# Kernel tuning notes

Hardware: AMD Instinct MI355X
Metric: run time of the kernel (lower is better)

The kernel has to match this reference:

```python
import jax, jax.numpy as jnp
import numpy as np

B, N, DIMS, K, UNITS = 4, 16384, 2, 16, 128
K1 = K + 1
CH = (DIMS + 1) * K1 + DIMS  # 53, matches ch_dims in LocSE.build
EPS = 1e-8


def setup_inputs() -> dict:
    key = jax.random.key(0)
    k1, k2, k3, k4 = jax.random.split(key, 4)
    pc = jax.random.normal(k1, (B, N, DIMS), jnp.float32)
    feats = jax.random.normal(k2, (B, N, UNITS // 2), jnp.float32)
    n_idx = jax.random.randint(k3, (B, N, K1), 0, N).astype(jnp.int32)
    W = jax.random.normal(k4, (CH, UNITS // 2), jnp.float32) * (1.0 / np.sqrt(CH))
    b = jnp.zeros((UNITS // 2,), jnp.float32)
    return {"pc": pc, "feats": feats, "n_idx": n_idx, "W": W, "b": b}


def _gather_neighbours(x, idx):
    # x: (B,N,C), idx: (B,N,K1) -> (B,N,K1,C); per-batch gather (batch_dims=1)
    return jax.vmap(lambda p, i: p[i])(x, idx)


def reference(pc, feats, n_idx, W, b):
    Bs, Ns, _ = pc.shape
    n_points = _gather_neighbours(pc, n_idx)                      # (B,N,K1,D)
    norms = jnp.linalg.norm(n_points, axis=-1, keepdims=True)     # (B,N,K1,1)
    # diff[b,n,j,i,:] = n_points[b,n,i,:] - n_points[b,n,j,:]  (i = 'current' loop index)
    diff = n_points[:, :, None, :, :] - n_points[:, :, :, None, :]  # (B,N,K1,K1,D)
    nb = jnp.broadcast_to(norms[:, :, :, None, :], diff.shape[:-1] + (1,))
    rpbns = jnp.concatenate([diff, nb], axis=-1)                  # (B,N,K1,K1,D+1)
    rpbns = rpbns.reshape(Bs, Ns, K1, K1 * (DIMS + 1))            # channel order: i*(D+1)+c
    rppe = jnp.concatenate([n_points, rpbns], axis=-1)            # (B,N,K1,CH)
    # pointwise Conv1D(kernel=1) MLP == dense over last axis
    r = jax.nn.relu(jnp.einsum('bnkc,cu->bnku', rppe, W) + b)     # (B,N,K1,UNITS//2)
    # global geometric features: linear-fit slope + pearson distance over neighbourhood
    x, y = n_points[..., 0], n_points[..., 1]
    mx = jnp.mean(x, axis=2, keepdims=True)
    my = jnp.mean(y, axis=2, keepdims=True)
    xc, yc = x - mx, y - my
    cov = jnp.mean(xc * yc, axis=2, keepdims=True)
    vx = jnp.mean(xc * xc, axis=2, keepdims=True)
    vy = jnp.mean(yc * yc, axis=2, keepdims=True)
    m = cov / (vx + EPS)                                          # slope of linear fit
    pear = cov / (jnp.sqrt(vx * vy) + EPS)
    ggf = jnp.stack([m, 1.0 - pear], axis=-1)                     # (B,N,1,2)
    n_feats = _gather_neighbours(feats, n_idx)                    # (B,N,K1,UNITS//2)
    out = jnp.concatenate([n_feats, r], axis=-1)                  # (B,N,K1,UNITS)
    return out, ggf
```

## Files before the change

kernel.cpp:

```cpp
#include <hip/hip_runtime.h>


#define NB 16384
#define K1C 17
#define UH 64

static constexpr long long OUT_R = 4LL * NB * K1C * 128;

__global__ __launch_bounds__(256) void locse_kernel(
    const float* __restrict__ pc,
    const float* __restrict__ feats,
    const int*   __restrict__ n_idx,
    const float* __restrict__ W,
    const float* __restrict__ bias,
    float* __restrict__ out)
{
    __shared__ float s_px[4][K1C];
    __shared__ float s_py[4][K1C];
    __shared__ float s_nr[4][K1C];
    __shared__ int   s_id[4][K1C];

    const int wave = threadIdx.x >> 6;
    const int lane = threadIdx.x & 63;
    const long long p = (long long)blockIdx.x * 4 + wave;
    const int bidx = (int)(p >> 14);

    if (lane < K1C) {
        int id = n_idx[p * K1C + lane];
        s_id[wave][lane] = id;
        const float* pp = pc + ((long long)bidx * NB + id) * 2;
        float x = pp[0];
        float y = pp[1];
        s_px[wave][lane] = x;
        s_py[wave][lane] = y;
        s_nr[wave][lane] = sqrtf(fmaf(x, x, y * y));
    }
    __syncthreads();

    const int u = lane;
    float w0 = W[u];
    float w1 = W[UH + u];
    const float* Wr = W + 2 * UH + u;

    float G = 0.f, swx = 0.f, swy = 0.f, swn = 0.f;
    float sx = 0.f, sy = 0.f, sxx = 0.f, syy = 0.f, sxy = 0.f;
#pragma unroll
    for (int i = 0; i < K1C; ++i) {
        float px = s_px[wave][i];
        float py = s_py[wave][i];
        float wx = Wr[(3 * i + 0) * UH];
        float wy = Wr[(3 * i + 1) * UH];
        float wn = Wr[(3 * i + 2) * UH];
        G = fmaf(px, wx, G);
        G = fmaf(py, wy, G);
        swx += wx; swy += wy; swn += wn;
        sx += px;  sy += py;
        sxx = fmaf(px, px, sxx);
        syy = fmaf(py, py, syy);
        sxy = fmaf(px, py, sxy);
    }
    float base = bias[u] + G;
    float c0 = w0 - swx;
    float c1 = w1 - swy;

    const long long fb = (long long)bidx * NB * UH;
    float* orow = out + p * (K1C * 128);
#pragma unroll
    for (int j = 0; j < K1C; ++j) {
        float v = fmaf(s_px[wave][j], c0,
                  fmaf(s_py[wave][j], c1,
                  fmaf(s_nr[wave][j], swn, base)));
        v = fmaxf(v, 0.f);
        float f = feats[fb + (long long)s_id[wave][j] * UH + u];
        orow[j * 128 + u]      = f;
        orow[j * 128 + UH + u] = v;
    }

    if (lane == 0) {
        const float inv = 1.0f / 17.0f;
        float mx = sx * inv, my = sy * inv;
        float cov = sxy * inv - mx * my;
        float vx = fmaxf(sxx * inv - mx * mx, 0.f);
        float vy = fmaxf(syy * inv - my * my, 0.f);
        float m = cov / (vx + 1e-8f);
        float pear = cov / (sqrtf(vx * vy) + 1e-8f);
        out[OUT_R + p * 2 + 0] = m;
        out[OUT_R + p * 2 + 1] = 1.0f - pear;
    }
}

extern "C" void kernel_launch(void* const* d_in, const int* in_sizes, int n_in,
                              void* d_out, int out_size, void* d_ws, size_t ws_size,
                              hipStream_t stream) {
    const float* pc    = (const float*)d_in[0];
    const float* feats = (const float*)d_in[1];
    const int*   n_idx = (const int*)d_in[2];
    const float* W     = (const float*)d_in[3];
    const float* bias  = (const float*)d_in[4];
    float* out = (float*)d_out;

    locse_kernel<<<16384, 256, 0, stream>>>(pc, feats, n_idx, W, bias, out);
}
```

Before: 619.9 us.

## Replace LDS staging with wave shuffles, prefetch feature gathers, interleave batch blocks

Drops the shared-memory staging and __syncthreads so each wave holds neighbour ids and coordinates in registers and broadcasts them with __shfl. All 17 feature-row gathers are issued up front into registers, giving more loads in flight. Blocks are remapped so consecutive blocks cycle over the four batches, which changes which gathered rows are live in cache at the same time. This uses more registers per thread and may lower occupancy.

Measured after the change: 623.3 us. Within noise of the previous version (+0.6%).

```diff
diff --git a/kernel.cpp b/kernel.cpp
--- a/kernel.cpp
+++ b/kernel.cpp
@@ -15,29 +15,29 @@
     const float* __restrict__ bias,
     float* __restrict__ out)
 {
-    __shared__ float s_px[4][K1C];
-    __shared__ float s_py[4][K1C];
-    __shared__ float s_nr[4][K1C];
-    __shared__ int   s_id[4][K1C];
-
     const int wave = threadIdx.x >> 6;
     const int lane = threadIdx.x & 63;
-    const long long p = (long long)blockIdx.x * 4 + wave;
-    const int bidx = (int)(p >> 14);
+    const int b = blockIdx.x & 3;
+    const int g = blockIdx.x >> 2;
+    const long long p = (long long)b * NB + g * 4 + wave;
 
-    if (lane < K1C) {
-        int id = n_idx[p * K1C + lane];
-        s_id[wave][lane] = id;
-        const float* pp = pc + ((long long)bidx * NB + id) * 2;
-        float x = pp[0];
-        float y = pp[1];
-        s_px[wave][lane] = x;
-        s_py[wave][lane] = y;
-        s_nr[wave][lane] = sqrtf(fmaf(x, x, y * y));
-    }
-    __syncthreads();
+    const int li = lane < K1C ? lane : K1C - 1;
+    const int id_l = n_idx[p * K1C + li];
+    const float2 pp = *(const float2*)(pc + ((long long)b * NB + id_l) * 2);
+    const float px_l = pp.x, py_l = pp.y;
+    const float nr_l = sqrtf(fmaf(pp.x, pp.x, pp.y * pp.y));
 
     const int u = lane;
+    const long long fb = (long long)b * NB * UH;
+
+    int ids[K1C];
+#pragma unroll
+    for (int j = 0; j < K1C; ++j) ids[j] = __shfl(id_l, j);
+    float fv[K1C];
+#pragma unroll
+    for (int j = 0; j < K1C; ++j)
+        fv[j] = feats[fb + (long long)ids[j] * UH + u];
+
     float w0 = W[u];
     float w1 = W[UH + u];
     const float* Wr = W + 2 * UH + u;
@@ -46,8 +46,8 @@
     float sx = 0.f, sy = 0.f, sxx = 0.f, syy = 0.f, sxy = 0.f;
 #pragma unroll
     for (int i = 0; i < K1C; ++i) {
-        float px = s_px[wave][i];
-        float py = s_py[wave][i];
+        float px = __shfl(px_l, i);
+        float py = __shfl(py_l, i);
         float wx = Wr[(3 * i + 0) * UH];
         float wy = Wr[(3 * i + 1) * UH];
         float wn = Wr[(3 * i + 2) * UH];
@@ -59,20 +59,18 @@
         syy = fmaf(py, py, syy);
         sxy = fmaf(px, py, sxy);
     }
-    float base = bias[u] + G;
-    float c0 = w0 - swx;
-    float c1 = w1 - swy;
+    const float base = bias[u] + G;
+    const float c0 = w0 - swx;
+    const float c1 = w1 - swy;
 
-    const long long fb = (long long)bidx * NB * UH;
     float* orow = out + p * (K1C * 128);
 #pragma unroll
     for (int j = 0; j < K1C; ++j) {
-        float v = fmaf(s_px[wave][j], c0,
-                  fmaf(s_py[wave][j], c1,
-                  fmaf(s_nr[wave][j], swn, base)));
-        v = fmaxf(v, 0.f);
-        float f = feats[fb + (long long)s_id[wave][j] * UH + u];
-        orow[j * 128 + u]      = f;
+        float px = __shfl(px_l, j);
+        float py = __shfl(py_l, j);
+        float nr = __shfl(nr_l, j);
+        float v = fmaxf(fmaf(px, c0, fmaf(py, c1, fmaf(nr, swn, base))), 0.f);
+        orow[j * 128 + u]      = fv[j];
         orow[j * 128 + UH + u] = v;
     }
 
```
